# Optimization experiments

Hardware: AMD Instinct MI355X
Metric: run time of the kernel (lower is better)

## Reference

```python
import jax, jax.numpy as jnp
import numpy as np

NEG_SLOPE = 0.2

def _gat_conv(x, W, att_src, att_dst, bias, src, dst, n_nodes):
    # x: [N, F_in], W: [F_in, F_out], att_*: [F_out], bias: [F_out]
    h = x @ W                                   # [N, F_out]
    a_src = h @ att_src                         # [N]
    a_dst = h @ att_dst                         # [N]
    e = a_src[src] + a_dst[dst]                 # [E]
    e = jnp.where(e > 0, e, NEG_SLOPE * e)      # LeakyReLU
    # segment softmax over incoming edges of each destination node
    m = jax.ops.segment_max(e, dst, num_segments=n_nodes)
    ex = jnp.exp(e - m[dst])
    denom = jax.ops.segment_sum(ex, dst, num_segments=n_nodes)
    alpha = ex / denom[dst]                     # [E]
    msg = alpha[:, None] * h[src]               # [E, F_out]
    out = jax.ops.segment_sum(msg, dst, num_segments=n_nodes)
    return out + bias

def setup_inputs() -> dict:
    key = jax.random.key(0)
    ks = jax.random.split(key, 12)
    N, E, F_in, H, F_out = 50000, 800000, 128, 128, 128
    def glorot(k, shape):
        lim = float(np.sqrt(6.0 / sum(shape))) if len(shape) > 1 else float(np.sqrt(6.0 / shape[0]))
        return jax.random.uniform(k, shape, jnp.float32, -lim, lim)
    return {
        "x": jax.random.normal(ks[0], (N, F_in), jnp.float32),
        "edge_index": jax.random.randint(ks[1], (2, E), 0, N, jnp.int64),
        "W1": glorot(ks[2], (F_in, H)),
        "att_src1": glorot(ks[3], (H,)),
        "att_dst1": glorot(ks[4], (H,)),
        "b1": jnp.zeros((H,), jnp.float32),
        "W2": glorot(ks[5], (H, F_out)),
        "att_src2": glorot(ks[6], (F_out,)),
        "att_dst2": glorot(ks[7], (F_out,)),
        "b2": jnp.zeros((F_out,), jnp.float32),
    }

def reference(x, edge_index, W1, att_src1, att_dst1, b1, W2, att_src2, att_dst2, b2):
    n_nodes = x.shape[0]
    # add self loops (PyG GATConv default)
    loops = jnp.arange(n_nodes, dtype=edge_index.dtype)
    src = jnp.concatenate([edge_index[0], loops])
    dst = jnp.concatenate([edge_index[1], loops])
    h = _gat_conv(x, W1, att_src1, att_dst1, b1, src, dst, n_nodes)
    h = jax.nn.relu(h)
    h = _gat_conv(h, W2, att_src2, att_dst2, b2, src, dst, n_nodes)
    return jax.nn.relu(h)
```

## Files before the change

kernel.cpp:

```cpp
#include <hip/hip_runtime.h>
#include <cstdint>

#define NEG_SLOPE 0.2f
#define F 128

#define BKT_SHIFT 7
#define BKT_SIZE  128
#define NBK_PAD   512
#define CHUNK     4096
#define EPT       8
#define CAP       3072

typedef unsigned short u16;
typedef unsigned int u32;
typedef float float8_t __attribute__((ext_vector_type(8)));
typedef float float4_t __attribute__((ext_vector_type(4)));
typedef short short8_t __attribute__((ext_vector_type(8)));

__device__ inline u16 f2bf(float f) {
    u32 u = __float_as_uint(f);
    u32 r = u + 0x7fffu + ((u >> 16) & 1u);
    return (u16)(r >> 16);
}
__device__ inline float bflo(u32 v) { return __uint_as_float(v << 16); }
__device__ inline float bfhi(u32 v) { return __uint_as_float(v & 0xffff0000u); }

__global__ void __launch_bounds__(512) bucket_count_kernel(const int* __restrict__ ei, int E, int tot,
                                                           int* __restrict__ bucketTotal) {
    __shared__ int hist[NBK_PAD];
    int tid = threadIdx.x;
    hist[tid] = 0;
    __syncthreads();
    int base = blockIdx.x * CHUNK;
    #pragma unroll
    for (int i = 0; i < EPT; ++i) {
        int e = base + i * 512 + tid;
        if (e < tot) {
            int d = (e < E) ? ei[E + e] : (e - E);
            atomicAdd(&hist[d >> BKT_SHIFT], 1);
        }
    }
    __syncthreads();
    int v = hist[tid];
    if (v > 0) atomicAdd(&bucketTotal[tid], v);
}

__global__ void __launch_bounds__(512) bucket_scan_kernel(const int* __restrict__ bucketTotal,
                                                          int* __restrict__ bucketStart,
                                                          int* __restrict__ bucketCursor) {
    __shared__ int sc[NBK_PAD];
    int t = threadIdx.x;
    int v = bucketTotal[t];
    sc[t] = v;
    __syncthreads();
    for (int o = 1; o < NBK_PAD; o <<= 1) {
        int u = (t >= o) ? sc[t - o] : 0;
        __syncthreads();
        sc[t] += u;
        __syncthreads();
    }
    int excl = sc[t] - v;
    bucketStart[t] = excl;
    bucketCursor[t] = excl;
    if (t == NBK_PAD - 1) bucketStart[NBK_PAD] = sc[t];
}

__global__ void __launch_bounds__(512) scatter_kernel(const int* __restrict__ ei, int E, int tot,
                                                      int* __restrict__ bucketCursor,
                                                      u32* __restrict__ pairs) {
    __shared__ int hist[NBK_PAD], excl[NBK_PAD], lcur[NBK_PAD], runb[NBK_PAD];
    __shared__ u32 stage[CHUNK];
    __shared__ u16 bktid[CHUNK];
    int tid = threadIdx.x;
    hist[tid] = 0;
    __syncthreads();
    int base = blockIdx.x * CHUNK;
    int chunkCnt = min(CHUNK, tot - base);
    int rs[EPT], rd[EPT];
    #pragma unroll
    for (int i = 0; i < EPT; ++i) {
        int e = base + i * 512 + tid;
        rd[i] = -1;
        if (e < tot) {
            int s, d;
            if (e < E) { s = ei[e]; d = ei[E + e]; } else { s = e - E; d = s; }
            rs[i] = s; rd[i] = d;
            atomicAdd(&hist[d >> BKT_SHIFT], 1);
        }
    }
    __syncthreads();
    int v = hist[tid];
    excl[tid] = v;
    __syncthreads();
    for (int o = 1; o < NBK_PAD; o <<= 1) {
        int u = (tid >= o) ? excl[tid - o] : 0;
        __syncthreads();
        excl[tid] += u;
        __syncthreads();
    }
    int ex = excl[tid] - v;
    __syncthreads();
    excl[tid] = ex;
    lcur[tid] = ex;
    if (v > 0) runb[tid] = atomicAdd(&bucketCursor[tid], v);
    __syncthreads();
    #pragma unroll
    for (int i = 0; i < EPT; ++i) {
        if (rd[i] >= 0) {
            int b = rd[i] >> BKT_SHIFT;
            int pos = atomicAdd(&lcur[b], 1);
            stage[pos] = ((u32)rs[i] << BKT_SHIFT) | (u32)(rd[i] & (BKT_SIZE - 1));
            bktid[pos] = (u16)b;
        }
    }
    __syncthreads();
    for (int j = tid; j < chunkCnt; j += 512) {
        int b = (int)bktid[j];
        pairs[(size_t)runb[b] + (j - excl[b])] = stage[j];
    }
}

__global__ void __launch_bounds__(256) build_kernel(const u32* __restrict__ pairs,
                                                    const int* __restrict__ bucketStart,
                                                    int* __restrict__ row_ptr, int* __restrict__ csr,
                                                    int N, int tot) {
    __shared__ u32 stage[CAP];
    __shared__ int sorted[CAP];
    __shared__ int hist[BKT_SIZE], pfx[BKT_SIZE], cur[BKT_SIZE];
    int b = blockIdx.x, tid = threadIdx.x;
    int base = bucketStart[b];
    int cnt = bucketStart[b + 1] - base;
    if (cnt > CAP) cnt = CAP;
    if (tid < BKT_SIZE) hist[tid] = 0;
    __syncthreads();
    for (int j = tid; j < cnt; j += 256) {
        u32 p = pairs[(size_t)base + j];
        stage[j] = p;
        atomicAdd(&hist[p & (BKT_SIZE - 1)], 1);
    }
    __syncthreads();
    if (tid < BKT_SIZE) pfx[tid] = hist[tid];
    __syncthreads();
    for (int o = 1; o < BKT_SIZE; o <<= 1) {
        int u = 0;
        if (tid < BKT_SIZE && tid >= o) u = pfx[tid - o];
        __syncthreads();
        if (tid < BKT_SIZE) pfx[tid] += u;
        __syncthreads();
    }
    if (tid < BKT_SIZE) {
        int ex = pfx[tid] - hist[tid];
        cur[tid] = ex;
        int d = b * BKT_SIZE + tid;
        if (d < N) row_ptr[d] = base + ex;
    }
    __syncthreads();
    for (int j = tid; j < cnt; j += 256) {
        u32 p = stage[j];
        int pos = atomicAdd(&cur[p & (BKT_SIZE - 1)], 1);
        sorted[pos] = (int)(p >> BKT_SHIFT);
    }
    __syncthreads();
    for (int j = tid; j < cnt; j += 256) csr[(size_t)base + j] = sorted[j];
    if (b == 0 && tid == 0) row_ptr[N] = tot;
}

__global__ void __launch_bounds__(256) prep_w_kernel(const float* __restrict__ W, u16* __restrict__ Wt) {
    int tid = threadIdx.x;
    #pragma unroll
    for (int j = 0; j < 8; ++j) {
        int u = tid + j * 256;
        int frag = u >> 6, lane = u & 63;
        int K0 = frag >> 3, nt = frag & 7;
        int kbase = K0 * 32 + (lane >> 4) * 8;
        int n = nt * 16 + (lane & 15);
        u32 w[4];
        #pragma unroll
        for (int p = 0; p < 4; ++p) {
            u16 e0 = f2bf(W[(size_t)(kbase + 2 * p) * F + n]);
            u16 e1 = f2bf(W[(size_t)(kbase + 2 * p + 1) * F + n]);
            w[p] = (u32)e0 | ((u32)e1 << 16);
        }
        uint4 o; o.x = w[0]; o.y = w[1]; o.z = w[2]; o.w = w[3];
        ((uint4*)Wt)[u] = o;
    }
}

template<int IN_BF16>
__global__ void __launch_bounds__(256) gemm_mfma_kernel(const void* __restrict__ in,
    const u16* __restrict__ Wt, const float* __restrict__ att_s, const float* __restrict__ att_d,
    u16* __restrict__ h, float* __restrict__ asrc, float* __restrict__ adst, int N)
{
    __shared__ u16 wlds[16384];
    int tid = threadIdx.x;
    {
        const uint4* src = (const uint4*)Wt;
        uint4* dst = (uint4*)wlds;
        #pragma unroll
        for (int i = 0; i < 8; ++i) dst[tid + i * 256] = src[tid + i * 256];
    }
    __syncthreads();
    int wave = tid >> 6, lane = tid & 63;
    int li = lane & 15, grp = lane >> 4;
    int rowBase = (blockIdx.x * 4 + wave) * 16;
    if (rowBase >= N) return;
    int row = rowBase + li;
    if (row > N - 1) row = N - 1;

    short8_t b[4];
    if (IN_BF16) {
        const u16* xp = (const u16*)in + (size_t)row * F + grp * 8;
        #pragma unroll
        for (int K0 = 0; K0 < 4; ++K0)
            b[K0] = *(const short8_t*)(xp + K0 * 32);
    } else {
        const float* xp = (const float*)in + (size_t)row * F + grp * 8;
        #pragma unroll
        for (int K0 = 0; K0 < 4; ++K0) {
            float8_t xv = *(const float8_t*)(xp + K0 * 32);
            short8_t t;
            #pragma unroll
            for (int i = 0; i < 8; ++i) t[i] = (short)f2bf(xv[i]);
            b[K0] = t;
        }
    }

    float4_t acc[8];
    #pragma unroll
    for (int nt = 0; nt < 8; ++nt) acc[nt] = (float4_t){0.f, 0.f, 0.f, 0.f};
    #pragma unroll
    for (int nt = 0; nt < 8; ++nt) {
        #pragma unroll
        for (int K0 = 0; K0 < 4; ++K0) {
            short8_t a = *(const short8_t*)&wlds[((K0 * 8 + nt) * 64 + lane) * 8];
            acc[nt] = __builtin_amdgcn_mfma_f32_16x16x32_bf16(a, b[K0], acc[nt], 0, 0, 0);
        }
    }

    u16* hr = h + (size_t)row * F + grp * 4;
    #pragma unroll
    for (int nt = 0; nt < 8; ++nt) {
        u32 lo = (u32)f2bf(acc[nt][0]) | ((u32)f2bf(acc[nt][1]) << 16);
        u32 hi = (u32)f2bf(acc[nt][2]) | ((u32)f2bf(acc[nt][3]) << 16);
        uint2 st; st.x = lo; st.y = hi;
        *(uint2*)(hr + (size_t)nt * 16) = st;
    }

    float rs = 0.f, rd = 0.f;
    #pragma unroll
    for (int nt = 0; nt < 8; ++nt) {
        float4 a4 = *(const float4*)(att_s + nt * 16 + grp * 4);
        float4 d4 = *(const float4*)(att_d + nt * 16 + grp * 4);
        rs += acc[nt][0] * a4.x + acc[nt][1] * a4.y + acc[nt][2] * a4.z + acc[nt][3] * a4.w;
        rd += acc[nt][0] * d4.x + acc[nt][1] * d4.y + acc[nt][2] * d4.z + acc[nt][3] * d4.w;
    }
    rs += __shfl_xor(rs, 16); rs += __shfl_xor(rs, 32);
    rd += __shfl_xor(rd, 16); rd += __shfl_xor(rd, 32);
    if (grp == 0) { asrc[row] = rs; adst[row] = rd; }
}

#define FMA8(pp, v)                                                              \
    acc[0] = fmaf(pp, bflo((v).x), acc[0]); acc[1] = fmaf(pp, bfhi((v).x), acc[1]); \
    acc[2] = fmaf(pp, bflo((v).y), acc[2]); acc[3] = fmaf(pp, bfhi((v).y), acc[3]); \
    acc[4] = fmaf(pp, bflo((v).z), acc[4]); acc[5] = fmaf(pp, bfhi((v).z), acc[5]); \
    acc[6] = fmaf(pp, bflo((v).w), acc[6]); acc[7] = fmaf(pp, bfhi((v).w), acc[7]);

template<int OUT_BF16>
__global__ void __launch_bounds__(256) aggregate_kernel(
    const u16* __restrict__ h, const float* __restrict__ asrc, const float* __restrict__ adst,
    const int* __restrict__ row_ptr, const int* __restrict__ csr,
    const float* __restrict__ bias, void* __restrict__ out, int N)
{
    int gid = blockIdx.x * 16 + (threadIdx.x >> 4);
    if (gid >= N) return;
    int lane = threadIdx.x & 15;
    int start = row_ptr[gid];
    int deg = row_ptr[gid + 1] - start;
    float ad = adst[gid];

    const uint4* h4 = (const uint4*)h;
    float denom = 0.f;
    float acc[8];
    #pragma unroll
    for (int j = 0; j < 8; ++j) acc[j] = 0.f;

    for (int c0 = 0; c0 < deg; c0 += 16) {
        int cnt = min(16, deg - c0);
        int s = 0; float p = 0.f;
        if (lane < cnt) {
            s = csr[start + c0 + lane];
            float e = asrc[s] + ad;
            e = (e > 0.f) ? e : NEG_SLOPE * e;
            p = __expf(fminf(e, 70.f));
        }
        denom += p;

        int t = 0;
        for (; t + 4 <= cnt; t += 4) {
            int s0 = __shfl(s, t, 16),     s1 = __shfl(s, t + 1, 16);
            int s2 = __shfl(s, t + 2, 16), s3 = __shfl(s, t + 3, 16);
            float p0 = __shfl(p, t, 16),     p1 = __shfl(p, t + 1, 16);
            float p2 = __shfl(p, t + 2, 16), p3 = __shfl(p, t + 3, 16);
            uint4 v0 = h4[(size_t)s0 * 16 + lane];
            uint4 v1 = h4[(size_t)s1 * 16 + lane];
            uint4 v2 = h4[(size_t)s2 * 16 + lane];
            uint4 v3 = h4[(size_t)s3 * 16 + lane];
            FMA8(p0, v0); FMA8(p1, v1); FMA8(p2, v2); FMA8(p3, v3);
        }
        for (; t < cnt; ++t) {
            int st = __shfl(s, t, 16);
            float pt = __shfl(p, t, 16);
            uint4 v = h4[(size_t)st * 16 + lane];
            FMA8(pt, v);
        }
    }

    #pragma unroll
    for (int o = 1; o < 16; o <<= 1) denom += __shfl_xor(denom, o);
    float inv = 1.0f / denom;
    const float* bp = bias + lane * 8;
    float r[8];
    #pragma unroll
    for (int j = 0; j < 8; ++j) {
        float v = fmaf(acc[j], inv, bp[j]);
        r[j] = v > 0.f ? v : 0.f;
    }
    if (OUT_BF16) {
        u32 w[4];
        #pragma unroll
        for (int p2 = 0; p2 < 4; ++p2)
            w[p2] = (u32)f2bf(r[2 * p2]) | ((u32)f2bf(r[2 * p2 + 1]) << 16);
        uint4 st; st.x = w[0]; st.y = w[1]; st.z = w[2]; st.w = w[3];
        ((uint4*)out)[(size_t)gid * 16 + lane] = st;
    } else {
        float4 o0 = make_float4(r[0], r[1], r[2], r[3]);
        float4 o1 = make_float4(r[4], r[5], r[6], r[7]);
        ((float4*)out)[(size_t)gid * 32 + lane * 2]     = o0;
        ((float4*)out)[(size_t)gid * 32 + lane * 2 + 1] = o1;
    }
}

static inline size_t align_up(size_t v, size_t a) { return (v + a - 1) & ~(a - 1); }

extern "C" void kernel_launch(void* const* d_in, const int* in_sizes, int n_in,
                              void* d_out, int out_size, void* d_ws, size_t ws_size,
                              hipStream_t stream) {
    const float* x   = (const float*)d_in[0];
    const int*   ei  = (const int*)d_in[1];
    const float* W1  = (const float*)d_in[2];
    const float* as1 = (const float*)d_in[3];
    const float* ad1 = (const float*)d_in[4];
    const float* b1  = (const float*)d_in[5];
    const float* W2  = (const float*)d_in[6];
    const float* as2 = (const float*)d_in[7];
    const float* ad2 = (const float*)d_in[8];
    const float* b2  = (const float*)d_in[9];

    int N = in_sizes[0] / F;
    int E = in_sizes[1] / 2;
    int tot = E + N;

    char* ws = (char*)d_ws;
    size_t off = 0;
    #define ALLOC(type, name, count)                                    \
        type* name = (type*)(ws + off);                                  \
        off = align_up(off + (size_t)(count) * sizeof(type), 256);
    ALLOC(u16,   h,       (size_t)N * F);
    ALLOC(u16,   out1,    (size_t)N * F);
    ALLOC(float, asrc,    N);
    ALLOC(float, adst,    N);
    ALLOC(int,   row_ptr, N + 4);
    ALLOC(int,   csr,     tot);
    ALLOC(u32,   pairs,   tot);
    ALLOC(int,   bucketTotal,  NBK_PAD);
    ALLOC(int,   bucketStart,  NBK_PAD + 1);
    ALLOC(int,   bucketCursor, NBK_PAD);
    ALLOC(u16,   Wt1,     16384);
    ALLOC(u16,   Wt2,     16384);
    #undef ALLOC

    hipMemsetAsync(bucketTotal, 0, NBK_PAD * sizeof(int), stream);

    int NBK = (N + BKT_SIZE - 1) / BKT_SIZE;
    int nchunks = (tot + CHUNK - 1) / CHUNK;

    prep_w_kernel<<<1, 256, 0, stream>>>(W1, Wt1);
    prep_w_kernel<<<1, 256, 0, stream>>>(W2, Wt2);

    bucket_count_kernel<<<nchunks, 512, 0, stream>>>(ei, E, tot, bucketTotal);
    bucket_scan_kernel<<<1, NBK_PAD, 0, stream>>>(bucketTotal, bucketStart, bucketCursor);
    scatter_kernel<<<nchunks, 512, 0, stream>>>(ei, E, tot, bucketCursor, pairs);
    build_kernel<<<NBK, 256, 0, stream>>>(pairs, bucketStart, row_ptr, csr, N, tot);

    int ngemm = (N + 63) / 64;
    int nagg  = (N + 15) / 16;

    gemm_mfma_kernel<0><<<ngemm, 256, 0, stream>>>(x, Wt1, as1, ad1, h, asrc, adst, N);
    aggregate_kernel<1><<<nagg, 256, 0, stream>>>(h, asrc, adst, row_ptr, csr, b1, out1, N);
    gemm_mfma_kernel<1><<<ngemm, 256, 0, stream>>>(out1, Wt2, as2, ad2, h, asrc, adst, N);
    aggregate_kernel<0><<<nagg, 256, 0, stream>>>(h, asrc, adst, row_ptr, csr, b2, d_out, N);
}
```

Measured before the change: 217.9 us.

## Merge preprocessing kernels, vectorize edge loads, co-launch CSR build with first GEMM

Folds both weight-prep launches into the bucket-count kernel as extra blocks, and co-launches the CSR build blocks with the first-layer GEMM blocks in one grid using shared LDS. The edge-index reads in count and scatter now use contiguous int4 loads per thread instead of strided scalar loads. The aggregation inner loop gains an 8-wide unrolled gather stage for more loads in flight. Together these aim to cut launch overhead and improve memory-level parallelism, at the cost of a 32KB LDS footprint for all fused-kernel blocks and more register pressure in aggregation.

```diff
diff --git a/kernel.cpp b/kernel.cpp
--- a/kernel.cpp
+++ b/kernel.cpp
@@ -25,19 +25,61 @@
 __device__ inline float bflo(u32 v) { return __uint_as_float(v << 16); }
 __device__ inline float bfhi(u32 v) { return __uint_as_float(v & 0xffff0000u); }
 
-__global__ void __launch_bounds__(512) bucket_count_kernel(const int* __restrict__ ei, int E, int tot,
-                                                           int* __restrict__ bucketTotal) {
+__device__ inline void prep_unit(const float* __restrict__ W, u16* __restrict__ Wt, int u) {
+    int frag = u >> 6, lane = u & 63;
+    int K0 = frag >> 3, nt = frag & 7;
+    int kbase = K0 * 32 + (lane >> 4) * 8;
+    int n = nt * 16 + (lane & 15);
+    u32 w[4];
+    #pragma unroll
+    for (int p = 0; p < 4; ++p) {
+        u16 e0 = f2bf(W[(size_t)(kbase + 2 * p) * F + n]);
+        u16 e1 = f2bf(W[(size_t)(kbase + 2 * p + 1) * F + n]);
+        w[p] = (u32)e0 | ((u32)e1 << 16);
+    }
+    uint4 o; o.x = w[0]; o.y = w[1]; o.z = w[2]; o.w = w[3];
+    ((uint4*)Wt)[u] = o;
+}
+
+__global__ void __launch_bounds__(512) count_prep_kernel(const int* __restrict__ ei, int E, int tot,
+                                                         int* __restrict__ bucketTotal,
+                                                         const float* __restrict__ W1, u16* __restrict__ Wt1,
+                                                         const float* __restrict__ W2, u16* __restrict__ Wt2,
+                                                         int nCountBlocks) {
+    if ((int)blockIdx.x >= nCountBlocks) {
+        int pb = blockIdx.x - nCountBlocks;
+        if (threadIdx.x < 512) {
+            int u = (pb & 3) * 512 + threadIdx.x;
+            if (pb < 4) prep_unit(W1, Wt1, u);
+            else        prep_unit(W2, Wt2, u);
+        }
+        return;
+    }
     __shared__ int hist[NBK_PAD];
     int tid = threadIdx.x;
     hist[tid] = 0;
     __syncthreads();
     int base = blockIdx.x * CHUNK;
-    #pragma unroll
-    for (int i = 0; i < EPT; ++i) {
-        int e = base + i * 512 + tid;
-        if (e < tot) {
-            int d = (e < E) ? ei[E + e] : (e - E);
-            atomicAdd(&hist[d >> BKT_SHIFT], 1);
+    int w = base + tid * EPT;
+    if (w + EPT <= E) {
+        int4 d0 = *(const int4*)&ei[E + w];
+        int4 d1 = *(const int4*)&ei[E + w + 4];
+        atomicAdd(&hist[d0.x >> BKT_SHIFT], 1);
+        atomicAdd(&hist[d0.y >> BKT_SHIFT], 1);
+        atomicAdd(&hist[d0.z >> BKT_SHIFT], 1);
+        atomicAdd(&hist[d0.w >> BKT_SHIFT], 1);
+        atomicAdd(&hist[d1.x >> BKT_SHIFT], 1);
+        atomicAdd(&hist[d1.y >> BKT_SHIFT], 1);
+        atomicAdd(&hist[d1.z >> BKT_SHIFT], 1);
+        atomicAdd(&hist[d1.w >> BKT_SHIFT], 1);
+    } else {
+        #pragma unroll
+        for (int i = 0; i < EPT; ++i) {
+            int e = w + i;
+            if (e < tot) {
+                int d = (e < E) ? ei[E + e] : (e - E);
+                atomicAdd(&hist[d >> BKT_SHIFT], 1);
+            }
         }
     }
     __syncthreads();
@@ -77,15 +119,29 @@
     int base = blockIdx.x * CHUNK;
     int chunkCnt = min(CHUNK, tot - base);
     int rs[EPT], rd[EPT];
-    #pragma unroll
-    for (int i = 0; i < EPT; ++i) {
-        int e = base + i * 512 + tid;
-        rd[i] = -1;
-        if (e < tot) {
-            int s, d;
-            if (e < E) { s = ei[e]; d = ei[E + e]; } else { s = e - E; d = s; }
-            rs[i] = s; rd[i] = d;
-            atomicAdd(&hist[d >> BKT_SHIFT], 1);
+    int w = base + tid * EPT;
+    if (w + EPT <= E) {
+        int4 s0 = *(const int4*)&ei[w];
+        int4 s1 = *(const int4*)&ei[w + 4];
+        int4 d0 = *(const int4*)&ei[E + w];
+        int4 d1 = *(const int4*)&ei[E + w + 4];
+        rs[0] = s0.x; rs[1] = s0.y; rs[2] = s0.z; rs[3] = s0.w;
+        rs[4] = s1.x; rs[5] = s1.y; rs[6] = s1.z; rs[7] = s1.w;
+        rd[0] = d0.x; rd[1] = d0.y; rd[2] = d0.z; rd[3] = d0.w;
+        rd[4] = d1.x; rd[5] = d1.y; rd[6] = d1.z; rd[7] = d1.w;
+        #pragma unroll
+        for (int i = 0; i < EPT; ++i) atomicAdd(&hist[rd[i] >> BKT_SHIFT], 1);
+    } else {
+        #pragma unroll
+        for (int i = 0; i < EPT; ++i) {
+            int e = w + i;
+            rd[i] = -1;
+            if (e < tot) {
+                int s, d;
+                if (e < E) { s = ei[e]; d = ei[E + e]; } else { s = e - E; d = s; }
+                rs[i] = s; rd[i] = d;
+                atomicAdd(&hist[d >> BKT_SHIFT], 1);
+            }
         }
     }
     __syncthreads();
@@ -120,14 +176,15 @@
     }
 }
 
-__global__ void __launch_bounds__(256) build_kernel(const u32* __restrict__ pairs,
-                                                    const int* __restrict__ bucketStart,
-                                                    int* __restrict__ row_ptr, int* __restrict__ csr,
-                                                    int N, int tot) {
-    __shared__ u32 stage[CAP];
-    __shared__ int sorted[CAP];
-    __shared__ int hist[BKT_SIZE], pfx[BKT_SIZE], cur[BKT_SIZE];
-    int b = blockIdx.x, tid = threadIdx.x;
+__device__ void build_body(const u32* __restrict__ pairs, const int* __restrict__ bucketStart,
+                           int* __restrict__ row_ptr, int* __restrict__ csr,
+                           int N, int tot, int b, char* smem) {
+    u32* stage  = (u32*)smem;
+    int* sorted = (int*)(smem + CAP * 4);
+    int* hist   = (int*)(smem + CAP * 8);
+    int* pfx    = (int*)(smem + CAP * 8 + 512);
+    int* cur    = (int*)(smem + CAP * 8 + 1024);
+    int tid = threadIdx.x;
     int base = bucketStart[b];
     int cnt = bucketStart[b + 1] - base;
     if (cnt > CAP) cnt = CAP;
@@ -165,25 +222,76 @@
     if (b == 0 && tid == 0) row_ptr[N] = tot;
 }
 
-__global__ void __launch_bounds__(256) prep_w_kernel(const float* __restrict__ W, u16* __restrict__ Wt) {
+template<int IN_BF16>
+__device__ void gemm_body(const void* __restrict__ in, const u16* __restrict__ Wt,
+                          const float* __restrict__ att_s, const float* __restrict__ att_d,
+                          u16* __restrict__ h, float* __restrict__ asrc, float* __restrict__ adst,
+                          int N, int gblk, u16* wlds) {
     int tid = threadIdx.x;
-    #pragma unroll
-    for (int j = 0; j < 8; ++j) {
-        int u = tid + j * 256;
-        int frag = u >> 6, lane = u & 63;
-        int K0 = frag >> 3, nt = frag & 7;
-        int kbase = K0 * 32 + (lane >> 4) * 8;
-        int n = nt * 16 + (lane & 15);
-        u32 w[4];
-        #pragma unroll
-        for (int p = 0; p < 4; ++p) {
-            u16 e0 = f2bf(W[(size_t)(kbase + 2 * p) * F + n]);
-            u16 e1 = f2bf(W[(size_t)(kbase + 2 * p + 1) * F + n]);
-            w[p] = (u32)e0 | ((u32)e1 << 16);
-        }
-        uint4 o; o.x = w[0]; o.y = w[1]; o.z = w[2]; o.w = w[3];
-        ((uint4*)Wt)[u] = o;
-    }
+    {
+        const uint4* src = (const uint4*)Wt;
+        uint4* dst = (uint4*)wlds;
+        #pragma unroll
+        for (int i = 0; i < 8; ++i) dst[tid + i * 256] = src[tid + i * 256];
+    }
+    __syncthreads();
+    int wave = tid >> 6, lane = tid & 63;
+    int li = lane & 15, grp = lane >> 4;
+    int rowBase = (gblk * 4 + wave) * 16;
+    if (rowBase >= N) return;
+    int row = rowBase + li;
+    if (row > N - 1) row = N - 1;
+
+    short8_t b[4];
+    if (IN_BF16) {
+        const u16* xp = (const u16*)in + (size_t)row * F + grp * 8;
+        #pragma unroll
+        for (int K0 = 0; K0 < 4; ++K0)
+            b[K0] = *(const short8_t*)(xp + K0 * 32);
+    } else {
+        const float* xp = (const float*)in + (size_t)row * F + grp * 8;
+        #pragma unroll
+        for (int K0 = 0; K0 < 4; ++K0) {
+            float8_t xv = *(const float8_t*)(xp + K0 * 32);
+            short8_t t;
+            #pragma unroll
+            for (int i = 0; i < 8; ++i) t[i] = (short)f2bf(xv[i]);
+            b[K0] = t;
+        }
+    }
+
+    float4_t acc[8];
+    #pragma unroll
+    for (int nt = 0; nt < 8; ++nt) acc[nt] = (float4_t){0.f, 0.f, 0.f, 0.f};
+    #pragma unroll
+    for (int nt = 0; nt < 8; ++nt) {
+        #pragma unroll
+        for (int K0 = 0; K0 < 4; ++K0) {
+            short8_t a = *(const short8_t*)&wlds[((K0 * 8 + nt) * 64 + lane) * 8];
+            acc[nt] = __builtin_amdgcn_mfma_f32_16x16x32_bf16(a, b[K0], acc[nt], 0, 0, 0);
+        }
+    }
+
+    u16* hr = h + (size_t)row * F + grp * 4;
+    #pragma unroll
+    for (int nt = 0; nt < 8; ++nt) {
+        u32 lo = (u32)f2bf(acc[nt][0]) | ((u32)f2bf(acc[nt][1]) << 16);
+        u32 hi = (u32)f2bf(acc[nt][2]) | ((u32)f2bf(acc[nt][3]) << 16);
+        uint2 st; st.x = lo; st.y = hi;
+        *(uint2*)(hr + (size_t)nt * 16) = st;
+    }
+
+    float rs = 0.f, rd = 0.f;
+    #pragma unroll
+    for (int nt = 0; nt < 8; ++nt) {
+        float4 a4 = *(const float4*)(att_s + nt * 16 + grp * 4);
+        float4 d4 = *(const float4*)(att_d + nt * 16 + grp * 4);
+        rs += acc[nt][0] * a4.x + acc[nt][1] * a4.y + acc[nt][2] * a4.z + acc[nt][3] * a4.w;
+        rd += acc[nt][0] * d4.x + acc[nt][1] * d4.y + acc[nt][2] * d4.z + acc[nt][3] * d4.w;
+    }
+    rs += __shfl_xor(rs, 16); rs += __shfl_xor(rs, 32);
+    rd += __shfl_xor(rd, 16); rd += __shfl_xor(rd, 32);
+    if (grp == 0) { asrc[row] = rs; adst[row] = rd; }
 }
 
 template<int IN_BF16>
@@ -192,71 +300,22 @@
     u16* __restrict__ h, float* __restrict__ asrc, float* __restrict__ adst, int N)
 {
     __shared__ u16 wlds[16384];
-    int tid = threadIdx.x;
-    {
-        const uint4* src = (const uint4*)Wt;
-        uint4* dst = (uint4*)wlds;
-        #pragma unroll
-        for (int i = 0; i < 8; ++i) dst[tid + i * 256] = src[tid + i * 256];
-    }
-    __syncthreads();
-    int wave = tid >> 6, lane = tid & 63;
-    int li = lane & 15, grp = lane >> 4;
-    int rowBase = (blockIdx.x * 4 + wave) * 16;
-    if (rowBase >= N) return;
-    int row = rowBase + li;
-    if (row > N - 1) row = N - 1;
-
-    short8_t b[4];
-    if (IN_BF16) {
-        const u16* xp = (const u16*)in + (size_t)row * F + grp * 8;
-        #pragma unroll
-        for (int K0 = 0; K0 < 4; ++K0)
-            b[K0] = *(const short8_t*)(xp + K0 * 32);
+    gemm_body<IN_BF16>(in, Wt, att_s, att_d, h, asrc, adst, N, blockIdx.x, wlds);
+}
+
+__global__ void __launch_bounds__(256) build_gemm_kernel(
+    const u32* __restrict__ pairs, const int* __restrict__ bucketStart,
+    int* __restrict__ row_ptr, int* __restrict__ csr, int N, int tot,
+    const float* __restrict__ x, const u16* __restrict__ Wt,
+    const float* __restrict__ att_s, const float* __restrict__ att_d,
+    u16* __restrict__ h, float* __restrict__ asrc, float* __restrict__ adst, int NBK)
+{
+    __shared__ __align__(16) char smem[32768];
+    if ((int)blockIdx.x < NBK) {
+        build_body(pairs, bucketStart, row_ptr, csr, N, tot, blockIdx.x, smem);
     } else {
-        const float* xp = (const float*)in + (size_t)row * F + grp * 8;
-        #pragma unroll
-        for (int K0 = 0; K0 < 4; ++K0) {
-            float8_t xv = *(const float8_t*)(xp + K0 * 32);
-            short8_t t;
-            #pragma unroll
-            for (int i = 0; i < 8; ++i) t[i] = (short)f2bf(xv[i]);
-            b[K0] = t;
-        }
-    }
-
-    float4_t acc[8];
-    #pragma unroll
-    for (int nt = 0; nt < 8; ++nt) acc[nt] = (float4_t){0.f, 0.f, 0.f, 0.f};
-    #pragma unroll
-    for (int nt = 0; nt < 8; ++nt) {
-        #pragma unroll
-        for (int K0 = 0; K0 < 4; ++K0) {
-            short8_t a = *(const short8_t*)&wlds[((K0 * 8 + nt) * 64 + lane) * 8];
-            acc[nt] = __builtin_amdgcn_mfma_f32_16x16x32_bf16(a, b[K0], acc[nt], 0, 0, 0);
-        }
-    }
-
-    u16* hr = h + (size_t)row * F + grp * 4;
-    #pragma unroll
-    for (int nt = 0; nt < 8; ++nt) {
-        u32 lo = (u32)f2bf(acc[nt][0]) | ((u32)f2bf(acc[nt][1]) << 16);
-        u32 hi = (u32)f2bf(acc[nt][2]) | ((u32)f2bf(acc[nt][3]) << 16);
-        uint2 st; st.x = lo; st.y = hi;
-        *(uint2*)(hr + (size_t)nt * 16) = st;
-    }
-
-    float rs = 0.f, rd = 0.f;
-    #pragma unroll
-    for (int nt = 0; nt < 8; ++nt) {
-        float4 a4 = *(const float4*)(att_s + nt * 16 + grp * 4);
-        float4 d4 = *(const float4*)(att_d + nt * 16 + grp * 4);
-        rs += acc[nt][0] * a4.x + acc[nt][1] * a4.y + acc[nt][2] * a4.z + acc[nt][3] * a4.w;
-        rd += acc[nt][0] * d4.x + acc[nt][1] * d4.y + acc[nt][2] * d4.z + acc[nt][3] * d4.w;
-    }
-    rs += __shfl_xor(rs, 16); rs += __shfl_xor(rs, 32);
-    rd += __shfl_xor(rd, 16); rd += __shfl_xor(rd, 32);
-    if (grp == 0) { asrc[row] = rs; adst[row] = rd; }
+        gemm_body<0>(x, Wt, att_s, att_d, h, asrc, adst, N, blockIdx.x - NBK, (u16*)smem);
+    }
 }
 
 #define FMA8(pp, v)                                                              \
@@ -296,6 +355,26 @@
         denom += p;
 
         int t = 0;
+        for (; t + 8 <= cnt; t += 8) {
+            int s0 = __shfl(s, t, 16),     s1 = __shfl(s, t + 1, 16);
+            int s2 = __shfl(s, t + 2, 16), s3 = __shfl(s, t + 3, 16);
+            int s4 = __shfl(s, t + 4, 16), s5 = __shfl(s, t + 5, 16);
+            int s6 = __shfl(s, t + 6, 16), s7 = __shfl(s, t + 7, 16);
+            float p0 = __shfl(p, t, 16),     p1 = __shfl(p, t + 1, 16);
+            float p2 = __shfl(p, t + 2, 16), p3 = __shfl(p, t + 3, 16);
+            float p4 = __shfl(p, t + 4, 16), p5 = __shfl(p, t + 5, 16);
+            float p6 = __shfl(p, t + 6, 16), p7 = __shfl(p, t + 7, 16);
+            uint4 v0 = h4[(size_t)s0 * 16 + lane];
+            uint4 v1 = h4[(size_t)s1 * 16 + lane];
+            uint4 v2 = h4[(size_t)s2 * 16 + lane];
+            uint4 v3 = h4[(size_t)s3 * 16 + lane];
+            uint4 v4 = h4[(size_t)s4 * 16 + lane];
+            uint4 v5 = h4[(size_t)s5 * 16 + lane];
+            uint4 v6 = h4[(size_t)s6 * 16 + lane];
+            uint4 v7 = h4[(size_t)s7 * 16 + lane];
+            FMA8(p0, v0); FMA8(p1, v1); FMA8(p2, v2); FMA8(p3, v3);
+            FMA8(p4, v4); FMA8(p5, v5); FMA8(p6, v6); FMA8(p7, v7);
+        }
         for (; t + 4 <= cnt; t += 4) {
             int s0 = __shfl(s, t, 16),     s1 = __shfl(s, t + 1, 16);
             int s2 = __shfl(s, t + 2, 16), s3 = __shfl(s, t + 3, 16);
@@ -383,19 +462,15 @@
 
     int NBK = (N + BKT_SIZE - 1) / BKT_SIZE;
     int nchunks = (tot + CHUNK - 1) / CHUNK;
-
-    prep_w_kernel<<<1, 256, 0, stream>>>(W1, Wt1);
-    prep_w_kernel<<<1, 256, 0, stream>>>(W2, Wt2);
-
-    bucket_count_kernel<<<nchunks, 512, 0, stream>>>(ei, E, tot, bucketTotal);
+    int ngemm = (N + 63) / 64;
+    int nagg  = (N + 15) / 16;
+
+    count_prep_kernel<<<nchunks + 8, 512, 0, stream>>>(ei, E, tot, bucketTotal,
+                                                       W1, Wt1, W2, Wt2, nchunks);
     bucket_scan_kernel<<<1, NBK_PAD, 0, stream>>>(bucketTotal, bucketStart, bucketCursor);
     scatter_kernel<<<nchunks, 512, 0, stream>>>(ei, E, tot, bucketCursor, pairs);
-    build_kernel<<<NBK, 256, 0, stream>>>(pairs, bucketStart, row_ptr, csr, N, tot);
-
-    int ngemm = (N + 63) / 64;
-    int nagg  = (N + 15) / 16;
-
-    gemm_mfma_kernel<0><<<ngemm, 256, 0, stream>>>(x, Wt1, as1, ad1, h, asrc, adst, N);
+    build_gemm_kernel<<<NBK + ngemm, 256, 0, stream>>>(pairs, bucketStart, row_ptr, csr, N, tot,
+                                                       x, Wt1, as1, ad1, h, asrc, adst, NBK);
     aggregate_kernel<1><<<nagg, 256, 0, stream>>>(h, asrc, adst, row_ptr, csr, b1, out1, N);
     gemm_mfma_kernel<1><<<ngemm, 256, 0, stream>>>(out1, Wt2, as2, ad2, h, asrc, adst, N);
     aggregate_kernel<0><<<nagg, 256, 0, stream>>>(h, asrc, adst, row_ptr, csr, b2, d_out, N);
```

Result: faster. 208.4 us (-4.4%).
